# Performance work log

Measured on AMD Instinct MI355X. Metric: run time of the kernel, lower is better.

Reference implementation:

```python
import jax, jax.numpy as jnp
import numpy as np

WL_W = 8   # wl_weight
WL_IN = 8  # wl_activate (input quantization)
EPS = 1e-5

def _wq(x, bits):
    # WAGE-style uniform quantize-dequantize to `bits` bits in [-1+step, 1-step], STE passthrough
    step = 2.0 ** (1 - bits)
    q = jnp.clip(jnp.round(x / step) * step, -1.0 + step, 1.0 - step)
    return x + jax.lax.stop_gradient(q - x)

def _qconv(x, w, b, pad):
    y = jax.lax.conv_general_dilated(
        _wq(x, WL_IN), _wq(w, WL_W), (1, 1), [(pad, pad), (pad, pad)],
        dimension_numbers=('NCHW', 'OIHW', 'NCHW'))
    return y + b[None, :, None, None]

def _bn_relu(x, g, be):
    # BatchNorm2d in training mode: batch statistics over (N, H, W)
    m = jnp.mean(x, axis=(0, 2, 3), keepdims=True)
    v = jnp.var(x, axis=(0, 2, 3), keepdims=True)
    return jax.nn.relu((x - m) * jax.lax.rsqrt(v + EPS) * g[None, :, None, None] + be[None, :, None, None])

def _maxpool3(x):
    # MaxPool2d(3, stride=1, padding=1)
    return jax.lax.reduce_window(x, -jnp.inf, jax.lax.max,
                                 (1, 1, 3, 3), (1, 1, 1, 1),
                                 [(0, 0), (0, 0), (1, 1), (1, 1)])

def setup_inputs() -> dict:
    key = jax.random.key(0)
    ks = jax.random.split(key, 8)
    d = {'x': jax.random.normal(ks[0], (128, 192, 32, 32), jnp.float32)}
    specs = [('b1', 1, 64, 192, 1), ('b2a', 2, 96, 192, 1), ('b2b', 3, 128, 96, 3),
             ('b3a', 4, 16, 192, 1), ('b3b', 5, 32, 16, 3), ('b3c', 6, 32, 32, 3),
             ('b4', 7, 32, 192, 1)]
    for name, i, co, ci, k in specs:
        d[name + '_w'] = jax.random.normal(ks[i], (co, ci, k, k), jnp.float32) * 0.05
        d[name + '_b'] = jnp.zeros((co,), jnp.float32)
        d[name + '_g'] = jnp.ones((co,), jnp.float32)
        d[name + '_be'] = jnp.zeros((co,), jnp.float32)
    return d

def reference(x,
              b1_w, b1_b, b1_g, b1_be,
              b2a_w, b2a_b, b2a_g, b2a_be,
              b2b_w, b2b_b, b2b_g, b2b_be,
              b3a_w, b3a_b, b3a_g, b3a_be,
              b3b_w, b3b_b, b3b_g, b3b_be,
              b3c_w, b3c_b, b3c_g, b3c_be,
              b4_w, b4_b, b4_g, b4_be):
    y1 = _bn_relu(_qconv(x, b1_w, b1_b, 0), b1_g, b1_be)
    y2 = _bn_relu(_qconv(x, b2a_w, b2a_b, 0), b2a_g, b2a_be)
    y2 = _bn_relu(_qconv(y2, b2b_w, b2b_b, 1), b2b_g, b2b_be)
    y3 = _bn_relu(_qconv(x, b3a_w, b3a_b, 0), b3a_g, b3a_be)
    y3 = _bn_relu(_qconv(y3, b3b_w, b3b_b, 1), b3b_g, b3b_be)
    y3 = _bn_relu(_qconv(y3, b3c_w, b3c_b, 1), b3c_g, b3c_be)
    y4 = _bn_relu(_qconv(_maxpool3(x), b4_w, b4_b, 0), b4_g, b4_be)
    return jnp.concatenate([y1, y2, y3, y4], axis=1)  # [N, 256, 32, 32]
```

## Files before the change

kernel.cpp:

```cpp
#include <hip/hip_runtime.h>

typedef unsigned short u16;
typedef unsigned int u32;
typedef __attribute__((ext_vector_type(4))) int i32x4;
typedef __attribute__((ext_vector_type(4))) float f32x4;
typedef __attribute__((ext_vector_type(4))) u16 u16x4;
typedef __attribute__((ext_vector_type(8))) u16 u16x8;

#define PTOT 131072
#define NREP 16

static __device__ __forceinline__ int qi8(float v) {
  int q = (int)rintf(v * 128.f);
  return max(-127, min(127, q));
}
static __device__ __forceinline__ u16 bf_rne(float v) {
  u32 u = __float_as_uint(v);
  u += 0x7fffu + ((u >> 16) & 1u);
  return (u16)(u >> 16);
}
static __device__ __forceinline__ float bf2f(u16 v) {
  return __uint_as_float((u32)v << 16);
}

struct WPtrs { const float* p[7]; };

__global__ void wpack_kernel(WPtrs wp, char* __restrict__ o) {
  static const int S[7][5] = {
      {0,      192, 192, 1, 64},
      {12288,  192, 192, 1, 96},
      {30720,  96,  320, 3, 128},
      {153600, 192, 192, 1, 16},
      {156672, 16,  64,  3, 32},
      {162816, 32,  128, 3, 32},
      {175104, 192, 192, 1, 32},
  };
  int idx = blockIdx.x * 256 + threadIdx.x;
  if (idx >= 181248) return;
  int s = 0;
#pragma unroll
  for (int i = 1; i < 7; ++i)
    if (idx >= S[i][0]) s = i;
  int local = idx - S[s][0];
  int CIr = S[s][1], KROWP = S[s][2], KH = S[s][3], Co = S[s][4];
  int j = local & 15, lane = (local >> 4) & 63, f = local >> 10;
  int NF = Co >> 4;
  int c = f / NF, nf = f - c * NF;
  int co = nf * 16 + (lane & 15);
  int k = c * 64 + ((lane >> 4) << 4) + j;
  int r = k / KROWP, kk = k - r * KROWP;
  char val = 0;
  if (kk < 3 * CIr || KH == 1) {
    int kw = (KH == 1) ? 0 : (kk / CIr);
    int ci = (KH == 1) ? kk : (kk - kw * CIr);
    val = (char)qi8(wp.p[s][(((size_t)co * CIr + ci) * KH + r) * KH + kw]);
  }
  o[idx] = val;
}

__global__ __launch_bounds__(256) void quantx_kernel(const float* __restrict__ x,
                                                     char* __restrict__ xq) {
  __shared__ __align__(16) char tile[64][80];
  int n = blockIdx.z, hwb = blockIdx.x * 64, cb = blockIdx.y * 64;
  int lane = threadIdx.x & 63, sub = threadIdx.x >> 6;
#pragma unroll
  for (int i = 0; i < 16; ++i) {
    int c = sub + i * 4;
    float v = x[(((size_t)n * 192 + cb + c) << 10) + hwb + lane];
    tile[lane][c] = (char)qi8(v);
  }
  __syncthreads();
  int t = threadIdx.x, px = t >> 2, c16 = t & 3;
  uint4 v = *(const uint4*)&tile[px][c16 * 16];
  *(uint4*)&xq[(((size_t)n << 10) + hwb + px) * 192 + cb + c16 * 16] = v;
}

template <int NFW, int MF>
static __device__ __forceinline__ void conv_epilogue(
    i32x4 (&acc)[MF][NFW], int nfw, int lane, int wave, int mbase,
    u16* __restrict__ yh, double* __restrict__ stb, int ststride) {
  float yv[MF][NFW][4];
#pragma unroll
  for (int mf = 0; mf < MF; ++mf)
#pragma unroll
    for (int nf = 0; nf < NFW; ++nf)
      if (nf < nfw) {
        int col = nf * 16 + (lane & 15);
        int pix = mbase + mf * 16 + ((lane >> 4) << 2);
        u16x4 o;
#pragma unroll
        for (int r = 0; r < 4; ++r) {
          float v = (float)acc[mf][nf][r] * 6.103515625e-05f;
          yv[mf][nf][r] = v;
          o[r] = bf_rne(v);
        }
        *(u16x4*)&yh[(size_t)col * PTOT + pix] = o;
      }

  float s1[NFW], s2[NFW];
#pragma unroll
  for (int nf = 0; nf < NFW; ++nf) { s1[nf] = 0.f; s2[nf] = 0.f; }
#pragma unroll
  for (int mf = 0; mf < MF; ++mf)
#pragma unroll
    for (int nf = 0; nf < NFW; ++nf)
      if (nf < nfw)
#pragma unroll
        for (int r = 0; r < 4; ++r) {
          float v = yv[mf][nf][r];
          s1[nf] += v;
          s2[nf] += v * v;
        }
#pragma unroll
  for (int m = 16; m <= 32; m <<= 1)
#pragma unroll
    for (int nf = 0; nf < NFW; ++nf) {
      s1[nf] += __shfl_xor(s1[nf], m);
      s2[nf] += __shfl_xor(s2[nf], m);
    }
  __shared__ float red[4][NFW][16][2];
  if (lane < 16)
#pragma unroll
    for (int nf = 0; nf < NFW; ++nf) {
      red[wave][nf][lane][0] = s1[nf];
      red[wave][nf][lane][1] = s2[nf];
    }
  __syncthreads();
  const int t = threadIdx.x;
  if (t < 16 * nfw) {
    int nf = t >> 4, l = t & 15;
    float a = red[0][nf][l][0] + red[1][nf][l][0] + red[2][nf][l][0] + red[3][nf][l][0];
    float b = red[0][nf][l][1] + red[1][nf][l][1] + red[2][nf][l][1] + red[3][nf][l][1];
    int rep = blockIdx.x & (NREP - 1);
    atomicAdd(&stb[rep * ststride + 2 * t], (double)a);
    atomicAdd(&stb[rep * ststride + 2 * t + 1], (double)b);
  }
}

__global__ __launch_bounds__(256, 4) void cstat1x1_kernel(
    const char* __restrict__ xq, const char* __restrict__ bpk,
    double* __restrict__ st, u16* __restrict__ yh) {
  constexpr int NFW = 6;
  constexpr int MF = 2;
  __shared__ __align__(16) char btile[18432];

  const int b = blockIdx.y;
  const int nfw = (b == 0) ? 4 : (b == 1) ? 6 : 1;
  const int bpo = (b == 0) ? 0 : (b == 1) ? 12288 : 153600;
  const int sto = (b == 0) ? 0 : (b == 1) ? 256 * NREP : 3 * 256 * NREP;
  const int yho = (b == 0) ? 0 : (b == 1) ? 64 : 160;
  const char* bp = bpk + bpo;
  double* stb = st + sto;
  u16* yhb = yh + (size_t)yho * PTOT;

  const int tid = threadIdx.x;
  const int bsz = nfw * 3 * 1024;
  for (int s = tid * 16; s < bsz; s += 4096)
    *(uint4*)&btile[s] = *(const uint4*)(bp + s);
  __syncthreads();

  const int lane = tid & 63;
  const int wave = tid >> 6;
  const int mbase = blockIdx.x * 128 + wave * 32;

  uint abase[MF];
#pragma unroll
  for (int mf = 0; mf < MF; ++mf)
    abase[mf] = (uint)(mbase + mf * 16 + (lane & 15)) * 192u;
  const uint klane = (uint)(lane >> 4) * 16u;
  const uint blane = (uint)lane * 16u;

  i32x4 acc[MF][NFW];
#pragma unroll
  for (int i = 0; i < MF; ++i)
#pragma unroll
    for (int j = 0; j < NFW; ++j) acc[i][j] = {0, 0, 0, 0};

#pragma unroll
  for (int c = 0; c < 3; ++c) {
    i32x4 af[MF];
#pragma unroll
    for (int mf = 0; mf < MF; ++mf)
      af[mf] = *(const i32x4*)(xq + (abase[mf] + (uint)c * 64u + klane));
    i32x4 bfr[NFW];
#pragma unroll
    for (int nf = 0; nf < NFW; ++nf)
      if (nf < nfw)
        bfr[nf] = *(const i32x4*)&btile[(uint)((c * nfw + nf) * 1024) + blane];
#pragma unroll
    for (int mf = 0; mf < MF; ++mf)
#pragma unroll
      for (int nf = 0; nf < NFW; ++nf)
        if (nf < nfw)
          acc[mf][nf] = __builtin_amdgcn_mfma_i32_16x16x64_i8(af[mf], bfr[nf],
                                                              acc[mf][nf], 0, 0, 0);
  }

  conv_epilogue<NFW, MF>(acc, nfw, lane, wave, mbase, yhb, stb, 256);
}

__global__ __launch_bounds__(256, 4) void cpool4_kernel(
    const char* __restrict__ xq, const char* __restrict__ bp,
    double* __restrict__ stb, u16* __restrict__ yh) {
  constexpr int NFW = 2;
  constexpr int MF = 2;
  __shared__ __align__(16) char pooled[128 * 192];
  __shared__ __align__(16) char btile[6144];

  const int tid = threadIdx.x;
  for (int s = tid * 16; s < 6144; s += 4096)
    *(uint4*)&btile[s] = *(const uint4*)(bp + s);

  const int p0 = blockIdx.x * 128;
  const int n = p0 >> 10, h0 = (p0 & 1023) >> 5;
  for (int task = tid; task < 128 * 12; task += 256) {
    int px = task / 12, c16 = task - px * 12;
    int h = h0 + (px >> 5), w = px & 31;
    int m[16];
#pragma unroll
    for (int j = 0; j < 16; ++j) m[j] = -127;
    for (int dh = -1; dh <= 1; ++dh) {
      int hh = h + dh; if (hh < 0 || hh > 31) continue;
      for (int dw = -1; dw <= 1; ++dw) {
        int ww = w + dw; if (ww < 0 || ww > 31) continue;
        uint4 v = *(const uint4*)&xq[((size_t)((n << 10) + (hh << 5) + ww)) * 192 +
                                     c16 * 16];
        const char* bb = reinterpret_cast<const char*>(&v);
#pragma unroll
        for (int t = 0; t < 16; ++t) {
          int b = (int)bb[t];
          m[t] = b > m[t] ? b : m[t];
        }
      }
    }
    uint4 o;
    char* ob = reinterpret_cast<char*>(&o);
#pragma unroll
    for (int t = 0; t < 16; ++t) ob[t] = (char)m[t];
    *(uint4*)&pooled[px * 192 + c16 * 16] = o;
  }
  __syncthreads();

  const int lane = tid & 63;
  const int wave = tid >> 6;
  const int mbase = blockIdx.x * 128 + wave * 32;

  uint albase[MF];
#pragma unroll
  for (int mf = 0; mf < MF; ++mf)
    albase[mf] = (uint)(wave * 32 + mf * 16 + (lane & 15)) * 192u;
  const uint klane = (uint)(lane >> 4) * 16u;
  const uint blane = (uint)lane * 16u;

  i32x4 acc[MF][NFW];
#pragma unroll
  for (int i = 0; i < MF; ++i)
#pragma unroll
    for (int j = 0; j < NFW; ++j) acc[i][j] = {0, 0, 0, 0};

#pragma unroll
  for (int c = 0; c < 3; ++c) {
    i32x4 af[MF];
#pragma unroll
    for (int mf = 0; mf < MF; ++mf)
      af[mf] = *(const i32x4*)&pooled[albase[mf] + (uint)c * 64u + klane];
    i32x4 bfr[NFW];
#pragma unroll
    for (int nf = 0; nf < NFW; ++nf)
      bfr[nf] = *(const i32x4*)&btile[(uint)((c * NFW + nf) * 1024) + blane];
#pragma unroll
    for (int mf = 0; mf < MF; ++mf)
#pragma unroll
      for (int nf = 0; nf < NFW; ++nf)
        acc[mf][nf] = __builtin_amdgcn_mfma_i32_16x16x64_i8(af[mf], bfr[nf],
                                                            acc[mf][nf], 0, 0, 0);
  }

  conv_epilogue<NFW, MF>(acc, NFW, lane, wave, mbase, yh, stb, 256);
}

template <int CI, int KROWP, int COB>
__global__ __launch_bounds__(256, 4) void cstat9q_kernel(
    const u16* __restrict__ yhin, const double* __restrict__ stp,
    const float* __restrict__ gp, const float* __restrict__ bep,
    const char* __restrict__ bp, int nft,
    double* __restrict__ stb, u16* __restrict__ yh) {
  constexpr int CPR = KROWP / 64;
  constexpr int NCH = 3 * CPR;
  constexpr int NFW = COB / 16;
  constexpr int MF = 2;
  constexpr int TILE = 6 * 34 * CI;
  constexpr int BSZ = NCH * NFW * 1024;

  __shared__ __align__(16) char atile[TILE + 64];
  __shared__ __align__(16) char btile[BSZ];
  __shared__ float2 cfl[CI];

  const int tid = threadIdx.x;

  if (tid < CI) {
    double s1d = 0., s2d = 0.;
#pragma unroll
    for (int r = 0; r < NREP; ++r) {
      s1d += stp[r * 256 + 2 * tid];
      s2d += stp[r * 256 + 2 * tid + 1];
    }
    double m = s1d * (1.0 / PTOT);
    double v = s2d * (1.0 / PTOT) - m * m;
    double inv = 1.0 / sqrt(v + 1e-5);
    double c0 = (double)gp[tid] * inv;
    cfl[tid] = make_float2((float)c0, (float)((double)bep[tid] - m * c0));
  }
  for (int s = tid * 16; s < BSZ; s += 4096)
    *(uint4*)&btile[s] = *(const uint4*)(bp + s);
  {
    uint4 z = {0, 0, 0, 0};
    for (int s = tid * 16; s < TILE + 64; s += 4096) *(uint4*)&atile[s] = z;
  }
  __syncthreads();

  const int p0 = blockIdx.x * 128;
  const int n = p0 >> 10, h0 = (p0 & 1023) >> 5;
  for (int task = tid; task < CI * 6; task += 256) {
    int co = task / 6, rr = task - co * 6;
    int irow = h0 - 1 + rr;
    if (irow < 0 || irow > 31) continue;
    const u16* src = yhin + (size_t)co * PTOT + (n << 10) + (irow << 5);
    float2 cc = cfl[co];
    char* dst = &atile[(rr * 34 + 1) * CI + co];
#pragma unroll
    for (int w8 = 0; w8 < 4; ++w8) {
      u16x8 v = *(const u16x8*)(src + w8 * 8);
#pragma unroll
      for (int e = 0; e < 8; ++e) {
        float z = fmaxf(fmaf(bf2f(v[e]), cc.x, cc.y), 0.f);
        dst[(w8 * 8 + e) * CI] = (char)min((int)rintf(z * 128.f), 127);
      }
    }
  }
  __syncthreads();

  const int lane = tid & 63;
  const int wave = tid >> 6;
  const int mbase = blockIdx.x * 128 + wave * 32;

  uint albase[MF];
#pragma unroll
  for (int mf = 0; mf < MF; ++mf) {
    int lp = wave * 32 + mf * 16 + (lane & 15);
    albase[mf] = (uint)((((lp >> 5) + 1) * 34 + 1 + (lp & 31)) * CI);
  }
  const uint klane = (uint)(lane >> 4) * 16u;
  const uint blane = (uint)lane * 16u;

  i32x4 acc[MF][NFW];
#pragma unroll
  for (int i = 0; i < MF; ++i)
#pragma unroll
    for (int j = 0; j < NFW; ++j) acc[i][j] = {0, 0, 0, 0};

#pragma unroll 2
  for (int c = 0; c < NCH; ++c) {
    int rr = c / CPR, o = (c - rr * CPR) * 64;
    uint koff = (uint)((rr - 1) * 34 * CI + o - CI);
    i32x4 af[MF];
#pragma unroll
    for (int mf = 0; mf < MF; ++mf)
      af[mf] = *(const i32x4*)&atile[albase[mf] + koff + klane];
    i32x4 bfr[NFW];
#pragma unroll
    for (int nf = 0; nf < NFW; ++nf)
      bfr[nf] = *(const i32x4*)&btile[(uint)((c * nft + nf) * 1024) + blane];
#pragma unroll
    for (int mf = 0; mf < MF; ++mf)
#pragma unroll
      for (int nf = 0; nf < NFW; ++nf)
        acc[mf][nf] = __builtin_amdgcn_mfma_i32_16x16x64_i8(af[mf], bfr[nf],
                                                            acc[mf][nf], 0, 0, 0);
  }

  conv_epilogue<NFW, MF>(acc, NFW, lane, wave, mbase, yh, stb, 256);
}

struct M2Args {
  const u16* yhin0; const double* stp0; const float* g0; const float* be0;
  const char* bp0; double* stb0; u16* yho0;
  const u16* yhin1; const double* stp1; const float* g1; const float* be1;
  const char* bp1; double* stb1; u16* yho1;
};

__global__ __launch_bounds__(256, 3) void cstat9m_kernel(M2Args A) {
  __shared__ __align__(16) char atile[6 * 34 * 96 + 64];
  __shared__ __align__(16) char btile[6144];
  __shared__ float2 cfl[96];
  __shared__ float redm[4][4][16][2];

  const int tid = threadIdx.x;

  if (blockIdx.y == 0) {
    constexpr int CI = 96;
    constexpr int CPR = 5;
    constexpr int NCH = 15;
    constexpr int MF = 4;
    constexpr int NFW = 4;
    constexpr int TILE = 6 * 34 * CI;

    if (tid < CI) {
      double s1d = 0., s2d = 0.;
#pragma unroll
      for (int r = 0; r < NREP; ++r) {
        s1d += A.stp0[r * 256 + 2 * tid];
        s2d += A.stp0[r * 256 + 2 * tid + 1];
      }
      double m = s1d * (1.0 / PTOT);
      double v = s2d * (1.0 / PTOT) - m * m;
      double inv = 1.0 / sqrt(v + 1e-5);
      double c0 = (double)A.g0[tid] * inv;
      cfl[tid] = make_float2((float)c0, (float)((double)A.be0[tid] - m * c0));
    }
    {
      uint4 z = {0, 0, 0, 0};
      for (int s = tid * 16; s < TILE + 64; s += 4096) *(uint4*)&atile[s] = z;
    }
    __syncthreads();

    const int p0 = blockIdx.x * 128;
    const int n = p0 >> 10, h0 = (p0 & 1023) >> 5;
    for (int task = tid; task < CI * 6; task += 256) {
      int co = task / 6, rr = task - co * 6;
      int irow = h0 - 1 + rr;
      if (irow < 0 || irow > 31) continue;
      const u16* src = A.yhin0 + (size_t)co * PTOT + (n << 10) + (irow << 5);
      float2 cc = cfl[co];
      char* dst = &atile[(rr * 34 + 1) * CI + co];
#pragma unroll
      for (int w8 = 0; w8 < 4; ++w8) {
        u16x8 v = *(const u16x8*)(src + w8 * 8);
#pragma unroll
        for (int e = 0; e < 8; ++e) {
          float z = fmaxf(fmaf(bf2f(v[e]), cc.x, cc.y), 0.f);
          dst[(w8 * 8 + e) * CI] = (char)min((int)rintf(z * 128.f), 127);
        }
      }
    }
    __syncthreads();

    const int lane = tid & 63;
    const int wave = tid >> 6;
    const int pg = wave >> 1, cg = wave & 1;

    uint albase[MF];
#pragma unroll
    for (int mf = 0; mf < MF; ++mf) {
      int lp = pg * 64 + mf * 16 + (lane & 15);
      albase[mf] = (uint)((((lp >> 5) + 1) * 34 + 1 + (lp & 31)) * CI);
    }
    const uint klane = (uint)(lane >> 4) * 16u;
    const uint blane = (uint)lane * 16u;

    i32x4 acc[MF][NFW];
#pragma unroll
    for (int i = 0; i < MF; ++i)
#pragma unroll
      for (int j = 0; j < NFW; ++j) acc[i][j] = {0, 0, 0, 0};

#pragma unroll 3
    for (int c = 0; c < NCH; ++c) {
      int rr = c / CPR, o = (c - rr * CPR) * 64;
      uint koff = (uint)((rr - 1) * 34 * CI + o - CI);
      i32x4 af[MF];
#pragma unroll
      for (int mf = 0; mf < MF; ++mf)
        af[mf] = *(const i32x4*)&atile[albase[mf] + koff + klane];
      i32x4 bfr[NFW];
#pragma unroll
      for (int nf = 0; nf < NFW; ++nf)
        bfr[nf] = *(const i32x4*)(A.bp0 +
                                  ((uint)((c * 8 + cg * 4 + nf) * 1024) + blane));
#pragma unroll
      for (int mf = 0; mf < MF; ++mf)
#pragma unroll
        for (int nf = 0; nf < NFW; ++nf)
          acc[mf][nf] = __builtin_amdgcn_mfma_i32_16x16x64_i8(af[mf], bfr[nf],
                                                              acc[mf][nf], 0, 0, 0);
    }

    float yv[MF][NFW][4];
#pragma unroll
    for (int mf = 0; mf < MF; ++mf)
#pragma unroll
      for (int nf = 0; nf < NFW; ++nf) {
        int col = cg * 64 + nf * 16 + (lane & 15);
        int pix = p0 + pg * 64 + mf * 16 + ((lane >> 4) << 2);
        u16x4 o;
#pragma unroll
        for (int r = 0; r < 4; ++r) {
          float v = (float)acc[mf][nf][r] * 6.103515625e-05f;
          yv[mf][nf][r] = v;
          o[r] = bf_rne(v);
        }
        *(u16x4*)&A.yho0[(size_t)col * PTOT + pix] = o;
      }

    float s1[NFW], s2[NFW];
#pragma unroll
    for (int nf = 0; nf < NFW; ++nf) { s1[nf] = 0.f; s2[nf] = 0.f; }
#pragma unroll
    for (int mf = 0; mf < MF; ++mf)
#pragma unroll
      for (int nf = 0; nf < NFW; ++nf)
#pragma unroll
        for (int r = 0; r < 4; ++r) {
          float v = yv[mf][nf][r];
          s1[nf] += v;
          s2[nf] += v * v;
        }
#pragma unroll
    for (int m = 16; m <= 32; m <<= 1)
#pragma unroll
      for (int nf = 0; nf < NFW; ++nf) {
        s1[nf] += __shfl_xor(s1[nf], m);
        s2[nf] += __shfl_xor(s2[nf], m);
      }
    if (lane < 16)
#pragma unroll
      for (int nf = 0; nf < NFW; ++nf) {
        redm[wave][nf][lane][0] = s1[nf];
        redm[wave][nf][lane][1] = s2[nf];
      }
    __syncthreads();
    if (tid < 128) {
      int gch = tid >> 4, l = tid & 15;
      int cg2 = gch >> 2, nf = gch & 3;
      float a = redm[cg2][nf][l][0] + redm[2 + cg2][nf][l][0];
      float b = redm[cg2][nf][l][1] + redm[2 + cg2][nf][l][1];
      int rep = blockIdx.x & (NREP - 1);
      atomicAdd(&A.stb0[rep * 256 + 2 * tid], (double)a);
      atomicAdd(&A.stb0[rep * 256 + 2 * tid + 1], (double)b);
    }
  } else {
    constexpr int CI = 16;
    constexpr int CPR = 1;
    constexpr int NCH = 3;
    constexpr int MF = 2;
    constexpr int NFW = 2;
    constexpr int TILE = 6 * 34 * CI;

    if (tid < CI) {
      double s1d = 0., s2d = 0.;
#pragma unroll
      for (int r = 0; r < NREP; ++r) {
        s1d += A.stp1[r * 256 + 2 * tid];
        s2d += A.stp1[r * 256 + 2 * tid + 1];
      }
      double m = s1d * (1.0 / PTOT);
      double v = s2d * (1.0 / PTOT) - m * m;
      double inv = 1.0 / sqrt(v + 1e-5);
      double c0 = (double)A.g1[tid] * inv;
      cfl[tid] = make_float2((float)c0, (float)((double)A.be1[tid] - m * c0));
    }
    for (int s = tid * 16; s < 6144; s += 4096)
      *(uint4*)&btile[s] = *(const uint4*)(A.bp1 + s);
    {
      uint4 z = {0, 0, 0, 0};
      for (int s = tid * 16; s < TILE + 64; s += 4096) *(uint4*)&atile[s] = z;
    }
    __syncthreads();

    const int p0 = blockIdx.x * 128;
    const int n = p0 >> 10, h0 = (p0 & 1023) >> 5;
    for (int task = tid; task < CI * 6; task += 256) {
      int co = task / 6, rr = task - co * 6;
      int irow = h0 - 1 + rr;
      if (irow < 0 || irow > 31) continue;
      const u16* src = A.yhin1 + (size_t)co * PTOT + (n << 10) + (irow << 5);
      float2 cc = cfl[co];
      char* dst = &atile[(rr * 34 + 1) * CI + co];
#pragma unroll
      for (int w8 = 0; w8 < 4; ++w8) {
        u16x8 v = *(const u16x8*)(src + w8 * 8);
#pragma unroll
        for (int e = 0; e < 8; ++e) {
          float z = fmaxf(fmaf(bf2f(v[e]), cc.x, cc.y), 0.f);
          dst[(w8 * 8 + e) * CI] = (char)min((int)rintf(z * 128.f), 127);
        }
      }
    }
    __syncthreads();

    const int lane = tid & 63;
    const int wave = tid >> 6;
    const int mbase = blockIdx.x * 128 + wave * 32;

    uint albase[MF];
#pragma unroll
    for (int mf = 0; mf < MF; ++mf) {
      int lp = wave * 32 + mf * 16 + (lane & 15);
      albase[mf] = (uint)((((lp >> 5) + 1) * 34 + 1 + (lp & 31)) * CI);
    }
    const uint klane = (uint)(lane >> 4) * 16u;
    const uint blane = (uint)lane * 16u;

    i32x4 acc[MF][NFW];
#pragma unroll
    for (int i = 0; i < MF; ++i)
#pragma unroll
      for (int j = 0; j < NFW; ++j) acc[i][j] = {0, 0, 0, 0};

#pragma unroll
    for (int c = 0; c < NCH; ++c) {
      int rr = c / CPR, o = (c - rr * CPR) * 64;
      uint koff = (uint)((rr - 1) * 34 * CI + o - CI);
      i32x4 af[MF];
#pragma unroll
      for (int mf = 0; mf < MF; ++mf)
        af[mf] = *(const i32x4*)&atile[albase[mf] + koff + klane];
      i32x4 bfr[NFW];
#pragma unroll
      for (int nf = 0; nf < NFW; ++nf)
        bfr[nf] = *(const i32x4*)&btile[(uint)((c * 2 + nf) * 1024) + blane];
#pragma unroll
      for (int mf = 0; mf < MF; ++mf)
#pragma unroll
        for (int nf = 0; nf < NFW; ++nf)
          acc[mf][nf] = __builtin_amdgcn_mfma_i32_16x16x64_i8(af[mf], bfr[nf],
                                                              acc[mf][nf], 0, 0, 0);
    }

    conv_epilogue<NFW, MF>(acc, NFW, lane, wave, mbase, A.yho1, A.stb1, 256);
  }
}

struct BnPtrs { const float* g[4]; const float* be[4]; };

__global__ __launch_bounds__(256) void bnout_all_kernel(
    const u16* __restrict__ yh, const double* __restrict__ st, BnPtrs bp,
    float* __restrict__ out) {
  int co = blockIdx.y, chunk = blockIdx.x, tid = threadIdx.x;
  int br = (co < 64) ? 0 : (co < 192) ? 1 : (co < 224) ? 2 : 3;
  int lco = co - ((br == 0) ? 0 : (br == 1) ? 64 : (br == 2) ? 192 : 224);
  int yhoff = (br == 0) ? 0 : (br == 1) ? 208 : (br == 2) ? 368 : 176;
  int stoff = (br == 0) ? 0 : (br == 1) ? 2 * 256 * NREP
                         : (br == 2) ? 5 * 256 * NREP : 6 * 256 * NREP;
  const double* stb = st + stoff;
  double s1d = 0., s2d = 0.;
#pragma unroll
  for (int r = 0; r < NREP; ++r) {
    s1d += stb[r * 256 + 2 * lco];
    s2d += stb[r * 256 + 2 * lco + 1];
  }
  double m = s1d * (1.0 / PTOT);
  double v = s2d * (1.0 / PTOT) - m * m;
  double inv = 1.0 / sqrt(v + 1e-5);
  double c0d = (double)bp.g[br][lco] * inv;
  float c0 = (float)c0d;
  float c1 = (float)((double)bp.be[br][lco] - m * c0d);

  int p0 = chunk * 4096 + tid * 16;
  int n = p0 >> 10, hw = p0 & 1023;
  const u16* yp = yh + (size_t)(yhoff + lco) * PTOT + p0;
  float* op = out + (((size_t)(n * 256 + co)) << 10) + hw;
#pragma unroll
  for (int half = 0; half < 2; ++half) {
    u16x8 r = *(const u16x8*)(yp + half * 8);
    f32x4 a, b;
#pragma unroll
    for (int e = 0; e < 4; ++e) {
      a[e] = fmaxf(fmaf(bf2f(r[e]), c0, c1), 0.f);
      b[e] = fmaxf(fmaf(bf2f(r[e + 4]), c0, c1), 0.f);
    }
    *(f32x4*)(op + half * 8) = a;
    *(f32x4*)(op + half * 8 + 4) = b;
  }
}

extern "C" void kernel_launch(void* const* d_in, const int* in_sizes, int n_in,
                              void* d_out, int out_size, void* d_ws, size_t ws_size,
                              hipStream_t stream) {
  const float* x = (const float*)d_in[0];
  float* out = (float*)d_out;
  char* ws = (char*)d_ws;

  if (ws_size < 155599872ull) return;
  char* xq  = ws;
  u16* yh   = (u16*)(ws + 50331648ull);
  char* bpk = ws + 155189248ull;
  double* st = (double*)(ws + 155370496ull);

  hipMemsetAsync(st, 0, 7 * NREP * 256 * 8, stream);

  WPtrs wp;
  const int widx[7] = {1, 5, 9, 13, 17, 21, 25};
  for (int i = 0; i < 7; ++i) wp.p[i] = (const float*)d_in[widx[i]];
  wpack_kernel<<<708, 256, 0, stream>>>(wp, bpk);

  quantx_kernel<<<dim3(16, 3, 128), 256, 0, stream>>>(x, xq);

  double* stB[7];
  for (int b = 0; b < 7; ++b) stB[b] = st + (size_t)b * NREP * 256;

  cpool4_kernel<<<1024, 256, 0, stream>>>(xq, bpk + 175104, stB[6],
                                          yh + (size_t)176 * PTOT);

  cstat1x1_kernel<<<dim3(1024, 3), 256, 0, stream>>>(xq, bpk, st, yh);

  M2Args A;
  A.yhin0 = yh + (size_t)64 * PTOT;  A.stp0 = stB[1];
  A.g0 = (const float*)d_in[7];      A.be0 = (const float*)d_in[8];
  A.bp0 = bpk + 30720;               A.stb0 = stB[2];
  A.yho0 = yh + (size_t)208 * PTOT;
  A.yhin1 = yh + (size_t)160 * PTOT; A.stp1 = stB[3];
  A.g1 = (const float*)d_in[15];     A.be1 = (const float*)d_in[16];
  A.bp1 = bpk + 156672;              A.stb1 = stB[4];
  A.yho1 = yh + (size_t)336 * PTOT;
  cstat9m_kernel<<<dim3(1024, 2), 256, 0, stream>>>(A);

  cstat9q_kernel<32, 128, 32><<<1024, 256, 0, stream>>>(
      yh + (size_t)336 * PTOT, stB[4], (const float*)d_in[19], (const float*)d_in[20],
      bpk + 162816, 2, stB[5], yh + (size_t)368 * PTOT);

  BnPtrs bp;
  bp.g[0] = (const float*)d_in[3];  bp.be[0] = (const float*)d_in[4];
  bp.g[1] = (const float*)d_in[11]; bp.be[1] = (const float*)d_in[12];
  bp.g[2] = (const float*)d_in[23]; bp.be[2] = (const float*)d_in[24];
  bp.g[3] = (const float*)d_in[27]; bp.be[3] = (const float*)d_in[28];
  bnout_all_kernel<<<dim3(32, 256), 256, 0, stream>>>(yh, st, bp, out);
}
```

Before: 186.3 us.

## Merge pool branch into 1x1 kernel and overlap BN output with later convs

Folds the maxpool+1x1 conv branch into the cstat1x1 launch as a fourth grid row, removing a separate launch. The final BN/ReLU write-out is split up: branches 1 and 4 are written by extra blocks of the cstat9m launch, branch 2 by extra blocks of the 3x3 branch-3 launch, and only branch 3 is left for a small final kernel. The aim is to fill idle CUs during the narrow conv kernels and cut launch count. In exchange, blocks in one grid now do very different amounts of work, and the 1x1 kernel's shared memory grows, which may lower occupancy.

```diff
diff --git a/kernel.cpp b/kernel.cpp
--- a/kernel.cpp
+++ b/kernel.cpp
@@ -75,6 +75,41 @@
   *(uint4*)&xq[(((size_t)n << 10) + hwb + px) * 192 + cb + c16 * 16] = v;
 }
 
+static __device__ __forceinline__ void bnout_one(
+    const u16* __restrict__ yhbase, const double* __restrict__ stb,
+    const float* __restrict__ g, const float* __restrict__ be,
+    float* __restrict__ out, int cog, int lco, int chunk, int tid) {
+  double s1d = 0., s2d = 0.;
+#pragma unroll
+  for (int r = 0; r < NREP; ++r) {
+    s1d += stb[r * 256 + 2 * lco];
+    s2d += stb[r * 256 + 2 * lco + 1];
+  }
+  double m = s1d * (1.0 / PTOT);
+  double v = s2d * (1.0 / PTOT) - m * m;
+  double inv = 1.0 / sqrt(v + 1e-5);
+  double c0d = (double)g[lco] * inv;
+  float c0 = (float)c0d;
+  float c1 = (float)((double)be[lco] - m * c0d);
+
+  int p0 = chunk * 4096 + tid * 16;
+  int n = p0 >> 10, hw = p0 & 1023;
+  const u16* yp = yhbase + (size_t)lco * PTOT + p0;
+  float* op = out + (((size_t)(n * 256 + cog + lco)) << 10) + hw;
+#pragma unroll
+  for (int half = 0; half < 2; ++half) {
+    u16x8 r = *(const u16x8*)(yp + half * 8);
+    f32x4 a, b;
+#pragma unroll
+    for (int e = 0; e < 4; ++e) {
+      a[e] = fmaxf(fmaf(bf2f(r[e]), c0, c1), 0.f);
+      b[e] = fmaxf(fmaf(bf2f(r[e + 4]), c0, c1), 0.f);
+    }
+    *(f32x4*)(op + half * 8) = a;
+    *(f32x4*)(op + half * 8 + 4) = b;
+  }
+}
+
 template <int NFW, int MF>
 static __device__ __forceinline__ void conv_epilogue(
     i32x4 (&acc)[MF][NFW], int nfw, int lane, int wave, int mbase,
@@ -142,31 +177,68 @@
     double* __restrict__ st, u16* __restrict__ yh) {
   constexpr int NFW = 6;
   constexpr int MF = 2;
-  __shared__ __align__(16) char btile[18432];
+  __shared__ __align__(16) char smem[30720];
 
   const int b = blockIdx.y;
-  const int nfw = (b == 0) ? 4 : (b == 1) ? 6 : 1;
-  const int bpo = (b == 0) ? 0 : (b == 1) ? 12288 : 153600;
-  const int sto = (b == 0) ? 0 : (b == 1) ? 256 * NREP : 3 * 256 * NREP;
-  const int yho = (b == 0) ? 0 : (b == 1) ? 64 : 160;
+  const int nfw = (b == 0) ? 4 : (b == 1) ? 6 : (b == 2) ? 1 : 2;
+  const int bpo = (b == 0) ? 0 : (b == 1) ? 12288 : (b == 2) ? 153600 : 175104;
+  const int sto = (b == 0) ? 0 : (b == 1) ? 256 * NREP
+                           : (b == 2) ? 3 * 256 * NREP : 6 * 256 * NREP;
+  const int yho = (b == 0) ? 0 : (b == 1) ? 64 : (b == 2) ? 160 : 176;
   const char* bp = bpk + bpo;
   double* stb = st + sto;
   u16* yhb = yh + (size_t)yho * PTOT;
 
   const int tid = threadIdx.x;
+  char* btile = smem;
+  char* pooled = smem + 6144;
   const int bsz = nfw * 3 * 1024;
   for (int s = tid * 16; s < bsz; s += 4096)
     *(uint4*)&btile[s] = *(const uint4*)(bp + s);
+
+  const int p0 = blockIdx.x * 128;
+  if (b == 3) {
+    const int n = p0 >> 10, h0 = (p0 & 1023) >> 5;
+    for (int task = tid; task < 128 * 12; task += 256) {
+      int px = task / 12, c16 = task - px * 12;
+      int h = h0 + (px >> 5), w = px & 31;
+      int m[16];
+#pragma unroll
+      for (int j = 0; j < 16; ++j) m[j] = -127;
+      for (int dh = -1; dh <= 1; ++dh) {
+        int hh = h + dh; if (hh < 0 || hh > 31) continue;
+        for (int dw = -1; dw <= 1; ++dw) {
+          int ww = w + dw; if (ww < 0 || ww > 31) continue;
+          uint4 v = *(const uint4*)&xq[((size_t)((n << 10) + (hh << 5) + ww)) * 192 +
+                                       c16 * 16];
+          const char* bb = reinterpret_cast<const char*>(&v);
+#pragma unroll
+          for (int t = 0; t < 16; ++t) {
+            int bv = (int)bb[t];
+            m[t] = bv > m[t] ? bv : m[t];
+          }
+        }
+      }
+      uint4 o;
+      char* ob = reinterpret_cast<char*>(&o);
+#pragma unroll
+      for (int t = 0; t < 16; ++t) ob[t] = (char)m[t];
+      *(uint4*)&pooled[px * 192 + c16 * 16] = o;
+    }
+  }
   __syncthreads();
 
   const int lane = tid & 63;
   const int wave = tid >> 6;
-  const int mbase = blockIdx.x * 128 + wave * 32;
-
-  uint abase[MF];
-#pragma unroll
-  for (int mf = 0; mf < MF; ++mf)
-    abase[mf] = (uint)(mbase + mf * 16 + (lane & 15)) * 192u;
+  const int mbase = p0 + wave * 32;
+
+  uint aoff[MF];
+#pragma unroll
+  for (int mf = 0; mf < MF; ++mf) {
+    int px = (b == 3) ? (wave * 32 + mf * 16 + (lane & 15))
+                      : (mbase + mf * 16 + (lane & 15));
+    aoff[mf] = (uint)px * 192u;
+  }
   const uint klane = (uint)(lane >> 4) * 16u;
   const uint blane = (uint)lane * 16u;
 
@@ -181,7 +253,8 @@
     i32x4 af[MF];
 #pragma unroll
     for (int mf = 0; mf < MF; ++mf)
-      af[mf] = *(const i32x4*)(xq + (abase[mf] + (uint)c * 64u + klane));
+      af[mf] = (b == 3) ? *(const i32x4*)&pooled[aoff[mf] + (uint)c * 64u + klane]
+                        : *(const i32x4*)(xq + (aoff[mf] + (uint)c * 64u + klane));
     i32x4 bfr[NFW];
 #pragma unroll
     for (int nf = 0; nf < NFW; ++nf)
@@ -197,189 +270,6 @@
   }
 
   conv_epilogue<NFW, MF>(acc, nfw, lane, wave, mbase, yhb, stb, 256);
-}
-
-__global__ __launch_bounds__(256, 4) void cpool4_kernel(
-    const char* __restrict__ xq, const char* __restrict__ bp,
-    double* __restrict__ stb, u16* __restrict__ yh) {
-  constexpr int NFW = 2;
-  constexpr int MF = 2;
-  __shared__ __align__(16) char pooled[128 * 192];
-  __shared__ __align__(16) char btile[6144];
-
-  const int tid = threadIdx.x;
-  for (int s = tid * 16; s < 6144; s += 4096)
-    *(uint4*)&btile[s] = *(const uint4*)(bp + s);
-
-  const int p0 = blockIdx.x * 128;
-  const int n = p0 >> 10, h0 = (p0 & 1023) >> 5;
-  for (int task = tid; task < 128 * 12; task += 256) {
-    int px = task / 12, c16 = task - px * 12;
-    int h = h0 + (px >> 5), w = px & 31;
-    int m[16];
-#pragma unroll
-    for (int j = 0; j < 16; ++j) m[j] = -127;
-    for (int dh = -1; dh <= 1; ++dh) {
-      int hh = h + dh; if (hh < 0 || hh > 31) continue;
-      for (int dw = -1; dw <= 1; ++dw) {
-        int ww = w + dw; if (ww < 0 || ww > 31) continue;
-        uint4 v = *(const uint4*)&xq[((size_t)((n << 10) + (hh << 5) + ww)) * 192 +
-                                     c16 * 16];
-        const char* bb = reinterpret_cast<const char*>(&v);
-#pragma unroll
-        for (int t = 0; t < 16; ++t) {
-          int b = (int)bb[t];
-          m[t] = b > m[t] ? b : m[t];
-        }
-      }
-    }
-    uint4 o;
-    char* ob = reinterpret_cast<char*>(&o);
-#pragma unroll
-    for (int t = 0; t < 16; ++t) ob[t] = (char)m[t];
-    *(uint4*)&pooled[px * 192 + c16 * 16] = o;
-  }
-  __syncthreads();
-
-  const int lane = tid & 63;
-  const int wave = tid >> 6;
-  const int mbase = blockIdx.x * 128 + wave * 32;
-
-  uint albase[MF];
-#pragma unroll
-  for (int mf = 0; mf < MF; ++mf)
-    albase[mf] = (uint)(wave * 32 + mf * 16 + (lane & 15)) * 192u;
-  const uint klane = (uint)(lane >> 4) * 16u;
-  const uint blane = (uint)lane * 16u;
-
-  i32x4 acc[MF][NFW];
-#pragma unroll
-  for (int i = 0; i < MF; ++i)
-#pragma unroll
-    for (int j = 0; j < NFW; ++j) acc[i][j] = {0, 0, 0, 0};
-
-#pragma unroll
-  for (int c = 0; c < 3; ++c) {
-    i32x4 af[MF];
-#pragma unroll
-    for (int mf = 0; mf < MF; ++mf)
-      af[mf] = *(const i32x4*)&pooled[albase[mf] + (uint)c * 64u + klane];
-    i32x4 bfr[NFW];
-#pragma unroll
-    for (int nf = 0; nf < NFW; ++nf)
-      bfr[nf] = *(const i32x4*)&btile[(uint)((c * NFW + nf) * 1024) + blane];
-#pragma unroll
-    for (int mf = 0; mf < MF; ++mf)
-#pragma unroll
-      for (int nf = 0; nf < NFW; ++nf)
-        acc[mf][nf] = __builtin_amdgcn_mfma_i32_16x16x64_i8(af[mf], bfr[nf],
-                                                            acc[mf][nf], 0, 0, 0);
-  }
-
-  conv_epilogue<NFW, MF>(acc, NFW, lane, wave, mbase, yh, stb, 256);
-}
-
-template <int CI, int KROWP, int COB>
-__global__ __launch_bounds__(256, 4) void cstat9q_kernel(
-    const u16* __restrict__ yhin, const double* __restrict__ stp,
-    const float* __restrict__ gp, const float* __restrict__ bep,
-    const char* __restrict__ bp, int nft,
-    double* __restrict__ stb, u16* __restrict__ yh) {
-  constexpr int CPR = KROWP / 64;
-  constexpr int NCH = 3 * CPR;
-  constexpr int NFW = COB / 16;
-  constexpr int MF = 2;
-  constexpr int TILE = 6 * 34 * CI;
-  constexpr int BSZ = NCH * NFW * 1024;
-
-  __shared__ __align__(16) char atile[TILE + 64];
-  __shared__ __align__(16) char btile[BSZ];
-  __shared__ float2 cfl[CI];
-
-  const int tid = threadIdx.x;
-
-  if (tid < CI) {
-    double s1d = 0., s2d = 0.;
-#pragma unroll
-    for (int r = 0; r < NREP; ++r) {
-      s1d += stp[r * 256 + 2 * tid];
-      s2d += stp[r * 256 + 2 * tid + 1];
-    }
-    double m = s1d * (1.0 / PTOT);
-    double v = s2d * (1.0 / PTOT) - m * m;
-    double inv = 1.0 / sqrt(v + 1e-5);
-    double c0 = (double)gp[tid] * inv;
-    cfl[tid] = make_float2((float)c0, (float)((double)bep[tid] - m * c0));
-  }
-  for (int s = tid * 16; s < BSZ; s += 4096)
-    *(uint4*)&btile[s] = *(const uint4*)(bp + s);
-  {
-    uint4 z = {0, 0, 0, 0};
-    for (int s = tid * 16; s < TILE + 64; s += 4096) *(uint4*)&atile[s] = z;
-  }
-  __syncthreads();
-
-  const int p0 = blockIdx.x * 128;
-  const int n = p0 >> 10, h0 = (p0 & 1023) >> 5;
-  for (int task = tid; task < CI * 6; task += 256) {
-    int co = task / 6, rr = task - co * 6;
-    int irow = h0 - 1 + rr;
-    if (irow < 0 || irow > 31) continue;
-    const u16* src = yhin + (size_t)co * PTOT + (n << 10) + (irow << 5);
-    float2 cc = cfl[co];
-    char* dst = &atile[(rr * 34 + 1) * CI + co];
-#pragma unroll
-    for (int w8 = 0; w8 < 4; ++w8) {
-      u16x8 v = *(const u16x8*)(src + w8 * 8);
-#pragma unroll
-      for (int e = 0; e < 8; ++e) {
-        float z = fmaxf(fmaf(bf2f(v[e]), cc.x, cc.y), 0.f);
-        dst[(w8 * 8 + e) * CI] = (char)min((int)rintf(z * 128.f), 127);
-      }
-    }
-  }
-  __syncthreads();
-
-  const int lane = tid & 63;
-  const int wave = tid >> 6;
-  const int mbase = blockIdx.x * 128 + wave * 32;
-
-  uint albase[MF];
-#pragma unroll
-  for (int mf = 0; mf < MF; ++mf) {
-    int lp = wave * 32 + mf * 16 + (lane & 15);
-    albase[mf] = (uint)((((lp >> 5) + 1) * 34 + 1 + (lp & 31)) * CI);
-  }
-  const uint klane = (uint)(lane >> 4) * 16u;
-  const uint blane = (uint)lane * 16u;
-
-  i32x4 acc[MF][NFW];
-#pragma unroll
-  for (int i = 0; i < MF; ++i)
-#pragma unroll
-    for (int j = 0; j < NFW; ++j) acc[i][j] = {0, 0, 0, 0};
-
-#pragma unroll 2
-  for (int c = 0; c < NCH; ++c) {
-    int rr = c / CPR, o = (c - rr * CPR) * 64;
-    uint koff = (uint)((rr - 1) * 34 * CI + o - CI);
-    i32x4 af[MF];
-#pragma unroll
-    for (int mf = 0; mf < MF; ++mf)
-      af[mf] = *(const i32x4*)&atile[albase[mf] + koff + klane];
-    i32x4 bfr[NFW];
-#pragma unroll
-    for (int nf = 0; nf < NFW; ++nf)
-      bfr[nf] = *(const i32x4*)&btile[(uint)((c * nft + nf) * 1024) + blane];
-#pragma unroll
-    for (int mf = 0; mf < MF; ++mf)
-#pragma unroll
-      for (int nf = 0; nf < NFW; ++nf)
-        acc[mf][nf] = __builtin_amdgcn_mfma_i32_16x16x64_i8(af[mf], bfr[nf],
-                                                            acc[mf][nf], 0, 0, 0);
-  }
-
-  conv_epilogue<NFW, MF>(acc, NFW, lane, wave, mbase, yh, stb, 256);
 }
 
 struct M2Args {
@@ -387,6 +277,8 @@
   const char* bp0; double* stb0; u16* yho0;
   const u16* yhin1; const double* stp1; const float* g1; const float* be1;
   const char* bp1; double* stb1; u16* yho1;
+  const u16* yh; const double* st; float* out;
+  const float* gb1; const float* beb1; const float* gb4; const float* beb4;
 };
 
 __global__ __launch_bounds__(256, 3) void cstat9m_kernel(M2Args A) {
@@ -396,8 +288,20 @@
   __shared__ float redm[4][4][16][2];
 
   const int tid = threadIdx.x;
-
-  if (blockIdx.y == 0) {
+  const int y = blockIdx.y;
+
+  if (y >= 2) {
+    int lco = ((y == 3) ? 32 : 0) + (blockIdx.x >> 5);
+    int chunk = blockIdx.x & 31;
+    if (y == 4)
+      bnout_one(A.yh + (size_t)176 * PTOT, A.st + 6 * 256 * NREP, A.gb4, A.beb4,
+                A.out, 224, lco, chunk, tid);
+    else
+      bnout_one(A.yh, A.st, A.gb1, A.beb1, A.out, 0, lco, chunk, tid);
+    return;
+  }
+
+  if (y == 0) {
     constexpr int CI = 96;
     constexpr int CPR = 5;
     constexpr int NCH = 15;
@@ -540,7 +444,6 @@
     }
   } else {
     constexpr int CI = 16;
-    constexpr int CPR = 1;
     constexpr int NCH = 3;
     constexpr int MF = 2;
     constexpr int NFW = 2;
@@ -609,8 +512,7 @@
 
 #pragma unroll
     for (int c = 0; c < NCH; ++c) {
-      int rr = c / CPR, o = (c - rr * CPR) * 64;
-      uint koff = (uint)((rr - 1) * 34 * CI + o - CI);
+      uint koff = (uint)((c - 1) * 34 * CI - CI);
       i32x4 af[MF];
 #pragma unroll
       for (int mf = 0; mf < MF; ++mf)
@@ -631,47 +533,124 @@
   }
 }
 
-struct BnPtrs { const float* g[4]; const float* be[4]; };
-
-__global__ __launch_bounds__(256) void bnout_all_kernel(
-    const u16* __restrict__ yh, const double* __restrict__ st, BnPtrs bp,
+struct M3Args {
+  const u16* yhin; const double* stp; const float* gp; const float* bep;
+  const char* bp; double* stb; u16* yho;
+  const u16* yh2b; const double* st2b; const float* g2b; const float* be2b;
+  float* out;
+};
+
+__global__ __launch_bounds__(256, 4) void cstat9c_kernel(M3Args A) {
+  constexpr int CI = 32;
+  constexpr int CPR = 2;
+  constexpr int NCH = 6;
+  constexpr int NFW = 2;
+  constexpr int MF = 2;
+  constexpr int TILE = 6 * 34 * CI;
+
+  __shared__ __align__(16) char atile[TILE + 64];
+  __shared__ __align__(16) char btile[12288];
+  __shared__ float2 cfl[CI];
+
+  const int tid = threadIdx.x;
+  const int y = blockIdx.y;
+
+  if (y >= 1) {
+    int lco = (y - 1) * 32 + (blockIdx.x >> 5);
+    int chunk = blockIdx.x & 31;
+    bnout_one(A.yh2b, A.st2b, A.g2b, A.be2b, A.out, 64, lco, chunk, tid);
+    return;
+  }
+
+  if (tid < CI) {
+    double s1d = 0., s2d = 0.;
+#pragma unroll
+    for (int r = 0; r < NREP; ++r) {
+      s1d += A.stp[r * 256 + 2 * tid];
+      s2d += A.stp[r * 256 + 2 * tid + 1];
+    }
+    double m = s1d * (1.0 / PTOT);
+    double v = s2d * (1.0 / PTOT) - m * m;
+    double inv = 1.0 / sqrt(v + 1e-5);
+    double c0 = (double)A.gp[tid] * inv;
+    cfl[tid] = make_float2((float)c0, (float)((double)A.bep[tid] - m * c0));
+  }
+  for (int s = tid * 16; s < 12288; s += 4096)
+    *(uint4*)&btile[s] = *(const uint4*)(A.bp + s);
+  {
+    uint4 z = {0, 0, 0, 0};
+    for (int s = tid * 16; s < TILE + 64; s += 4096) *(uint4*)&atile[s] = z;
+  }
+  __syncthreads();
+
+  const int p0 = blockIdx.x * 128;
+  const int n = p0 >> 10, h0 = (p0 & 1023) >> 5;
+  for (int task = tid; task < CI * 6; task += 256) {
+    int co = task / 6, rr = task - co * 6;
+    int irow = h0 - 1 + rr;
+    if (irow < 0 || irow > 31) continue;
+    const u16* src = A.yhin + (size_t)co * PTOT + (n << 10) + (irow << 5);
+    float2 cc = cfl[co];
+    char* dst = &atile[(rr * 34 + 1) * CI + co];
+#pragma unroll
+    for (int w8 = 0; w8 < 4; ++w8) {
+      u16x8 v = *(const u16x8*)(src + w8 * 8);
+#pragma unroll
+      for (int e = 0; e < 8; ++e) {
+        float z = fmaxf(fmaf(bf2f(v[e]), cc.x, cc.y), 0.f);
+        dst[(w8 * 8 + e) * CI] = (char)min((int)rintf(z * 128.f), 127);
+      }
+    }
+  }
+  __syncthreads();
+
+  const int lane = tid & 63;
+  const int wave = tid >> 6;
+  const int mbase = blockIdx.x * 128 + wave * 32;
+
+  uint albase[MF];
+#pragma unroll
+  for (int mf = 0; mf < MF; ++mf) {
+    int lp = wave * 32 + mf * 16 + (lane & 15);
+    albase[mf] = (uint)((((lp >> 5) + 1) * 34 + 1 + (lp & 31)) * CI);
+  }
+  const uint klane = (uint)(lane >> 4) * 16u;
+  const uint blane = (uint)lane * 16u;
+
+  i32x4 acc[MF][NFW];
+#pragma unroll
+  for (int i = 0; i < MF; ++i)
+#pragma unroll
+    for (int j = 0; j < NFW; ++j) acc[i][j] = {0, 0, 0, 0};
+
+#pragma unroll 2
+  for (int c = 0; c < NCH; ++c) {
+    int rr = c / CPR, o = (c - rr * CPR) * 64;
+    uint koff = (uint)((rr - 1) * 34 * CI + o - CI);
+    i32x4 af[MF];
+#pragma unroll
+    for (int mf = 0; mf < MF; ++mf)
+      af[mf] = *(const i32x4*)&atile[albase[mf] + koff + klane];
+    i32x4 bfr[NFW];
+#pragma unroll
+    for (int nf = 0; nf < NFW; ++nf)
+      bfr[nf] = *(const i32x4*)&btile[(uint)((c * 2 + nf) * 1024) + blane];
+#pragma unroll
+    for (int mf = 0; mf < MF; ++mf)
+#pragma unroll
+      for (int nf = 0; nf < NFW; ++nf)
+        acc[mf][nf] = __builtin_amdgcn_mfma_i32_16x16x64_i8(af[mf], bfr[nf],
+                                                            acc[mf][nf], 0, 0, 0);
+  }
+
+  conv_epilogue<NFW, MF>(acc, NFW, lane, wave, mbase, A.yho, A.stb, 256);
+}
+
+__global__ __launch_bounds__(256) void bnout_fin_kernel(
+    const u16* __restrict__ yh, const double* __restrict__ st,
+    const float* __restrict__ g, const float* __restrict__ be,
     float* __restrict__ out) {
-  int co = blockIdx.y, chunk = blockIdx.x, tid = threadIdx.x;
-  int br = (co < 64) ? 0 : (co < 192) ? 1 : (co < 224) ? 2 : 3;
-  int lco = co - ((br == 0) ? 0 : (br == 1) ? 64 : (br == 2) ? 192 : 224);
-  int yhoff = (br == 0) ? 0 : (br == 1) ? 208 : (br == 2) ? 368 : 176;
-  int stoff = (br == 0) ? 0 : (br == 1) ? 2 * 256 * NREP
-                         : (br == 2) ? 5 * 256 * NREP : 6 * 256 * NREP;
-  const double* stb = st + stoff;
-  double s1d = 0., s2d = 0.;
-#pragma unroll
-  for (int r = 0; r < NREP; ++r) {
-    s1d += stb[r * 256 + 2 * lco];
-    s2d += stb[r * 256 + 2 * lco + 1];
-  }
-  double m = s1d * (1.0 / PTOT);
-  double v = s2d * (1.0 / PTOT) - m * m;
-  double inv = 1.0 / sqrt(v + 1e-5);
-  double c0d = (double)bp.g[br][lco] * inv;
-  float c0 = (float)c0d;
-  float c1 = (float)((double)bp.be[br][lco] - m * c0d);
-
-  int p0 = chunk * 4096 + tid * 16;
-  int n = p0 >> 10, hw = p0 & 1023;
-  const u16* yp = yh + (size_t)(yhoff + lco) * PTOT + p0;
-  float* op = out + (((size_t)(n * 256 + co)) << 10) + hw;
-#pragma unroll
-  for (int half = 0; half < 2; ++half) {
-    u16x8 r = *(const u16x8*)(yp + half * 8);
-    f32x4 a, b;
-#pragma unroll
-    for (int e = 0; e < 4; ++e) {
-      a[e] = fmaxf(fmaf(bf2f(r[e]), c0, c1), 0.f);
-      b[e] = fmaxf(fmaf(bf2f(r[e + 4]), c0, c1), 0.f);
-    }
-    *(f32x4*)(op + half * 8) = a;
-    *(f32x4*)(op + half * 8 + 4) = b;
-  }
+  bnout_one(yh, st, g, be, out, 192, blockIdx.y, blockIdx.x, threadIdx.x);
 }
 
 extern "C" void kernel_launch(void* const* d_in, const int* in_sizes, int n_in,
@@ -699,10 +678,7 @@
   double* stB[7];
   for (int b = 0; b < 7; ++b) stB[b] = st + (size_t)b * NREP * 256;
 
-  cpool4_kernel<<<1024, 256, 0, stream>>>(xq, bpk + 175104, stB[6],
-                                          yh + (size_t)176 * PTOT);
-
-  cstat1x1_kernel<<<dim3(1024, 3), 256, 0, stream>>>(xq, bpk, st, yh);
+  cstat1x1_kernel<<<dim3(1024, 4), 256, 0, stream>>>(xq, bpk, st, yh);
 
   M2Args A;
   A.yhin0 = yh + (size_t)64 * PTOT;  A.stp0 = stB[1];
@@ -713,16 +689,22 @@
   A.g1 = (const float*)d_in[15];     A.be1 = (const float*)d_in[16];
   A.bp1 = bpk + 156672;              A.stb1 = stB[4];
   A.yho1 = yh + (size_t)336 * PTOT;
-  cstat9m_kernel<<<dim3(1024, 2), 256, 0, stream>>>(A);
-
-  cstat9q_kernel<32, 128, 32><<<1024, 256, 0, stream>>>(
-      yh + (size_t)336 * PTOT, stB[4], (const float*)d_in[19], (const float*)d_in[20],
-      bpk + 162816, 2, stB[5], yh + (size_t)368 * PTOT);
-
-  BnPtrs bp;
-  bp.g[0] = (const float*)d_in[3];  bp.be[0] = (const float*)d_in[4];
-  bp.g[1] = (const float*)d_in[11]; bp.be[1] = (const float*)d_in[12];
-  bp.g[2] = (const float*)d_in[23]; bp.be[2] = (const float*)d_in[24];
-  bp.g[3] = (const float*)d_in[27]; bp.be[3] = (const float*)d_in[28];
-  bnout_all_kernel<<<dim3(32, 256), 256, 0, stream>>>(yh, st, bp, out);
-}
+  A.yh = yh; A.st = st; A.out = out;
+  A.gb1 = (const float*)d_in[3];     A.beb1 = (const float*)d_in[4];
+  A.gb4 = (const float*)d_in[27];    A.beb4 = (const float*)d_in[28];
+  cstat9m_kernel<<<dim3(1024, 5), 256, 0, stream>>>(A);
+
+  M3Args C;
+  C.yhin = yh + (size_t)336 * PTOT;  C.stp = stB[4];
+  C.gp = (const float*)d_in[19];     C.bep = (const float*)d_in[20];
+  C.bp = bpk + 162816;               C.stb = stB[5];
+  C.yho = yh + (size_t)368 * PTOT;
+  C.yh2b = yh + (size_t)208 * PTOT;  C.st2b = stB[2];
+  C.g2b = (const float*)d_in[11];    C.be2b = (const float*)d_in[12];
+  C.out = out;
+  cstat9c_kernel<<<dim3(1024, 5), 256, 0, stream>>>(C);
+
+  bnout_fin_kernel<<<dim3(32, 32), 256, 0, stream>>>(
+      yh + (size_t)368 * PTOT, stB[5], (const float*)d_in[23],
+      (const float*)d_in[24], out);
+}
```

Result: no change. 188.7 us (+1.3%).
